# Performance work log

Hardware: AMD Instinct MI355X
Metric: run time of the kernel (lower is better)

Reference implementation:

```python
import jax, jax.numpy as jnp
import numpy as np

D_MODEL = 1024
D_HEAD = 128


def setup_inputs() -> dict:
    key = jax.random.key(0)
    kx, kq, kk, kv, ko = jax.random.split(key, 5)
    x = jax.random.normal(kx, (4, 2048, D_MODEL), dtype=jnp.float32)
    # xavier-uniform-ish init scale
    s_in = (6.0 / (D_MODEL + D_HEAD)) ** 0.5
    wq = jax.random.uniform(kq, (D_MODEL, D_HEAD), minval=-s_in, maxval=s_in, dtype=jnp.float32)
    wk = jax.random.uniform(kk, (D_MODEL, D_HEAD), minval=-s_in, maxval=s_in, dtype=jnp.float32)
    wv = jax.random.uniform(kv, (D_MODEL, D_HEAD), minval=-s_in, maxval=s_in, dtype=jnp.float32)
    wo = jax.random.uniform(ko, (D_HEAD, D_MODEL), minval=-s_in, maxval=s_in, dtype=jnp.float32)
    return {"x": x, "wq": wq, "wk": wk, "wv": wv, "wo": wo}


def reference(x, wq, wk, wv, wo):
    # x: [b, s, d_model]
    s = x.shape[1]
    scale = 1.0 / (D_HEAD ** 0.5)
    q = jnp.einsum('bsd,dh->bsh', x, wq)
    k = jnp.einsum('bsd,dh->bsh', x, wk)
    v = jnp.einsum('bsd,dh->bsh', x, wv)
    scores = jnp.einsum('bqh,bkh->bqk', q, k) * scale  # [b, s, s]
    causal = jnp.tril(jnp.ones((s, s), dtype=bool))
    scores = jnp.where(causal, scores, -jnp.inf)
    attn = jax.nn.softmax(scores, axis=-1)
    ctx = jnp.einsum('bqk,bkh->bqh', attn, v)
    return jnp.einsum('bsh,hd->bsd', ctx, wo)
```

## Files before the change

kernel.cpp:

```cpp
#include <hip/hip_runtime.h>
#include <hip/hip_bf16.h>
#include <math.h>

typedef _Float16 half8 __attribute__((ext_vector_type(8)));
typedef _Float16 half4_t __attribute__((ext_vector_type(4)));
typedef _Float16 half2_t __attribute__((ext_vector_type(2)));
typedef float floatx4 __attribute__((ext_vector_type(4)));
typedef float floatx2 __attribute__((ext_vector_type(2)));

#define MFMA16(a, b, c) __builtin_amdgcn_mfma_f32_16x16x32_f16(a, b, c, 0, 0, 0)
#define MASKVAL (-30000.0f)
#define QSCALE 0.1275261529f

__global__ __launch_bounds__(256) void wprep(
    const float* __restrict__ wq, const float* __restrict__ wk,
    const float* __restrict__ wv, const float* __restrict__ wo,
    _Float16* __restrict__ wqt, _Float16* __restrict__ wkt,
    _Float16* __restrict__ wvt, _Float16* __restrict__ wot) {
  __shared__ float T[32][36];
  int bx = blockIdx.x, tid = threadIdx.x;
  const float* src;
  _Float16* dst;
  int R, C, r0, c0;
  float sc = 1.0f;
  if (bx < 384) {
    int p = bx >> 7, t = bx & 127;
    src = (p == 0) ? wq : (p == 1) ? wk : wv;
    dst = (p == 0) ? wqt : (p == 1) ? wkt : wvt;
    if (p == 0) sc = QSCALE;
    R = 1024; C = 128;
    r0 = (t & 31) * 32; c0 = (t >> 5) * 32;
  } else {
    int t = bx - 384;
    src = wo; dst = wot;
    R = 128; C = 1024;
    r0 = (t & 3) * 32; c0 = (t >> 2) * 32;
  }
  {
    int row = tid >> 3, c4 = (tid & 7) * 4;
    float4 f = *(const float4*)&src[(size_t)(r0 + row) * C + c0 + c4];
    T[row][c4] = f.x; T[row][c4 + 1] = f.y; T[row][c4 + 2] = f.z; T[row][c4 + 3] = f.w;
  }
  __syncthreads();
  {
    int cc = tid >> 3, r4 = (tid & 7) * 4;
    half4_t h;
    h[0] = (_Float16)(T[r4 + 0][cc] * sc);
    h[1] = (_Float16)(T[r4 + 1][cc] * sc);
    h[2] = (_Float16)(T[r4 + 2][cc] * sc);
    h[3] = (_Float16)(T[r4 + 3][cc] * sc);
    *(half4_t*)&dst[(size_t)(c0 + cc) * R + r0 + r4] = h;
  }
}

__global__ __launch_bounds__(256) void qkv_gemm(
    const float* __restrict__ x, const _Float16* __restrict__ wqt,
    const _Float16* __restrict__ wkt, const _Float16* __restrict__ wvt,
    _Float16* __restrict__ Qh, _Float16* __restrict__ Kh,
    _Float16* __restrict__ Vt) {
  __shared__ _Float16 A_lds[32 * 72];
  __shared__ _Float16 B_lds[128 * 72];
  int tid = threadIdx.x;
  int w = tid >> 6, lane = tid & 63, quad = lane >> 4, l16 = lane & 15;
  int m0 = blockIdx.x * 32;
  int proj = blockIdx.y;
  const _Float16* wt = (proj == 0) ? wqt : (proj == 1) ? wkt : wvt;
  floatx4 zero = {0.f, 0.f, 0.f, 0.f};
  floatx4 acc[4];
#pragma unroll
  for (int t = 0; t < 4; t++) acc[t] = zero;

  int arow = tid >> 3, ak8 = (tid & 7) * 8;
  int brow = tid >> 1, bk32 = (tid & 1) * 32;
  int mw = (w >> 1) * 16, nw = (w & 1) * 64;

  for (int k0 = 0; k0 < 1024; k0 += 64) {
    {
      const float* s = x + (size_t)(m0 + arow) * 1024 + k0 + ak8;
      float4 f0 = *(const float4*)(s);
      float4 f1 = *(const float4*)(s + 4);
      half8 h;
      h[0] = (_Float16)f0.x; h[1] = (_Float16)f0.y; h[2] = (_Float16)f0.z; h[3] = (_Float16)f0.w;
      h[4] = (_Float16)f1.x; h[5] = (_Float16)f1.y; h[6] = (_Float16)f1.z; h[7] = (_Float16)f1.w;
      *(half8*)&A_lds[arow * 72 + ak8] = h;
    }
#pragma unroll
    for (int i = 0; i < 4; i++)
      *(half8*)&B_lds[brow * 72 + bk32 + i * 8] =
          *(const half8*)&wt[(size_t)brow * 1024 + k0 + bk32 + i * 8];
    __syncthreads();
    half8 a[2];
#pragma unroll
    for (int c = 0; c < 2; c++)
      a[c] = *(const half8*)&A_lds[(mw + l16) * 72 + c * 32 + quad * 8];
#pragma unroll
    for (int t = 0; t < 4; t++)
#pragma unroll
      for (int c = 0; c < 2; c++) {
        half8 b = *(const half8*)&B_lds[(nw + t * 16 + l16) * 72 + c * 32 + quad * 8];
        acc[t] = MFMA16(a[c], b, acc[t]);
      }
    __syncthreads();
  }
#pragma unroll
  for (int t = 0; t < 4; t++)
#pragma unroll
    for (int r = 0; r < 4; r++) {
      int row = m0 + mw + quad * 4 + r;
      int col = nw + t * 16 + l16;
      _Float16 v = (_Float16)acc[t][r];
      if (proj == 0)
        Qh[(size_t)row * 128 + col] = v;
      else if (proj == 1)
        Kh[(size_t)row * 128 + col] = v;
      else {
        int bb = row >> 11, s = row & 2047;
        Vt[((size_t)(bb * 128 + col)) * 2048 + s] = v;
      }
    }
}

__global__ __launch_bounds__(256, 3) void attn_partial(
    const _Float16* __restrict__ Qh, const _Float16* __restrict__ Kh,
    const _Float16* __restrict__ Vt, _Float16* __restrict__ Opart,
    float* __restrict__ Ml) {
  __shared__ _Float16 KV_lds[128 * 136];
  __shared__ _Float16 P_lds[4 * 16 * 136];
  int tid = threadIdx.x;
  int w = tid >> 6, lane = tid & 63, quad = lane >> 4, l16 = lane & 15;
  int g = (int)blockIdx.x;
  int b = g & 3;
  int r = 271 - (g >> 2);
  int m = (int)sqrtf((float)r + 1.0f);
  while (m * (m + 1) > r) m--;
  while ((m + 1) * (m + 2) <= r) m++;
  int s1 = (m + 1) * (m + 1);
  int qt, kc;
  if (r >= s1) { qt = 2 * m + 1; kc = r - s1; }
  else         { qt = 2 * m;     kc = r - m * (m + 1); }
  int q0 = qt * 64, k0 = kc * 128;
  int qw0 = q0 + w * 16;
  int sidx = (b * 32 + qt) * 16 + kc;

  const _Float16* Kb = Kh + (size_t)b * 2048 * 128;
  const _Float16* Vb = Vt + (size_t)b * 128 * 2048;

  int srow = tid >> 1, scol = (tid & 1) * 64;
#pragma unroll
  for (int i = 0; i < 8; i++)
    *(half8*)&KV_lds[srow * 136 + scol + i * 8] =
        *(const half8*)&Kb[(size_t)(k0 + srow) * 128 + scol + i * 8];
  half8 vreg[8];
#pragma unroll
  for (int i = 0; i < 8; i++)
    vreg[i] = *(const half8*)&Vb[(size_t)srow * 2048 + k0 + scol + i * 8];

  half8 aq[4];
  {
    const _Float16* qbase = Qh + (size_t)(b * 2048 + qw0 + l16) * 128;
#pragma unroll
    for (int c = 0; c < 4; c++) aq[c] = *(const half8*)&qbase[c * 32 + quad * 8];
  }
  __syncthreads();

  floatx4 zero = {0.f, 0.f, 0.f, 0.f};
  floatx4 sa[8];
#pragma unroll
  for (int t = 0; t < 8; t++) sa[t] = zero;
#pragma unroll
  for (int t = 0; t < 8; t++)
#pragma unroll
    for (int c = 0; c < 4; c++) {
      half8 bk = *(const half8*)&KV_lds[(t * 16 + l16) * 136 + c * 32 + quad * 8];
      sa[t] = MFMA16(aq[c], bk, sa[t]);
    }

  float m_r[4], l_r[4];
#pragma unroll
  for (int r2 = 0; r2 < 4; r2++) {
    int query = qw0 + quad * 4 + r2;
    float mx = MASKVAL;
#pragma unroll
    for (int t = 0; t < 8; t++) {
      float s = (k0 + t * 16 + l16 > query) ? MASKVAL : sa[t][r2];
      sa[t][r2] = s;
      mx = fmaxf(mx, s);
    }
#pragma unroll
    for (int off = 1; off < 16; off <<= 1) mx = fmaxf(mx, __shfl_xor(mx, off));
    float rs = 0.f;
#pragma unroll
    for (int t = 0; t < 8; t++) {
      float e = exp2f(sa[t][r2] - mx);
      sa[t][r2] = e;
      rs += e;
    }
#pragma unroll
    for (int off = 1; off < 16; off <<= 1) rs += __shfl_xor(rs, off);
    m_r[r2] = mx;
    l_r[r2] = rs;
  }

  __syncthreads();

#pragma unroll
  for (int i = 0; i < 8; i++)
    *(half8*)&KV_lds[srow * 136 + scol + i * 8] = vreg[i];
  _Float16* P = P_lds + w * 16 * 136;
#pragma unroll
  for (int r2 = 0; r2 < 4; r2++)
#pragma unroll
    for (int t = 0; t < 8; t++)
      P[(quad * 4 + r2) * 136 + t * 16 + l16] = (_Float16)sa[t][r2];
  __syncthreads();

  floatx4 O[8];
#pragma unroll
  for (int t = 0; t < 8; t++) O[t] = zero;
#pragma unroll
  for (int c2 = 0; c2 < 4; c2++) {
    half8 ap = *(const half8*)&P[l16 * 136 + c2 * 32 + quad * 8];
#pragma unroll
    for (int t = 0; t < 8; t++) {
      half8 bv = *(const half8*)&KV_lds[(t * 16 + l16) * 136 + c2 * 32 + quad * 8];
      O[t] = MFMA16(ap, bv, O[t]);
    }
  }

  size_t obase = (size_t)sidx * 8192;
#pragma unroll
  for (int t = 0; t < 8; t++)
#pragma unroll
    for (int r2 = 0; r2 < 4; r2++)
      Opart[obase + (size_t)(w * 16 + quad * 4 + r2) * 128 + t * 16 + l16] = (_Float16)O[t][r2];
  if (l16 == 0)
#pragma unroll
    for (int r2 = 0; r2 < 4; r2++) {
      int row = w * 16 + quad * 4 + r2;
      floatx2 ml;
      ml[0] = m_r[r2];
      ml[1] = l_r[r2];
      *(floatx2*)&Ml[(size_t)sidx * 128 + row * 2] = ml;
    }
}

__global__ __launch_bounds__(256) void attn_combine(
    const _Float16* __restrict__ Opart, const float* __restrict__ Ml,
    _Float16* __restrict__ ctx) {
  int tid = threadIdx.x;
  int w = tid >> 6, lane = tid & 63;
  int row = blockIdx.x * 4 + w;
  int b = row >> 11, s = row & 2047;
  int qt = s >> 6, ri = s & 63;
  int nkc = (qt + 2) >> 1;
  int sidx0 = (b * 32 + qt) * 16;
  float M = MASKVAL;
  for (int i = 0; i < nkc; i++)
    M = fmaxf(M, Ml[(size_t)(sidx0 + i) * 128 + ri * 2]);
  float L = 0.f, a0 = 0.f, a1 = 0.f;
  for (int i = 0; i < nkc; i++) {
    float mi = Ml[(size_t)(sidx0 + i) * 128 + ri * 2];
    float li = Ml[(size_t)(sidx0 + i) * 128 + ri * 2 + 1];
    float sc = exp2f(mi - M);
    L += li * sc;
    half2_t o = *(const half2_t*)&Opart[(size_t)(sidx0 + i) * 8192 + (size_t)ri * 128 + lane * 2];
    a0 += sc * (float)o[0];
    a1 += sc * (float)o[1];
  }
  float inv = 1.f / L;
  half2_t hv;
  hv[0] = (_Float16)(a0 * inv);
  hv[1] = (_Float16)(a1 * inv);
  *(half2_t*)&ctx[(size_t)row * 128 + lane * 2] = hv;
}

__global__ __launch_bounds__(256) void out_gemm(
    const _Float16* __restrict__ ctx, const _Float16* __restrict__ wot,
    float* __restrict__ out) {
  __shared__ _Float16 A_lds[64 * 136];
  __shared__ _Float16 B_lds[128 * 136];
  int tid = threadIdx.x;
  int w = tid >> 6, lane = tid & 63, quad = lane >> 4, l16 = lane & 15;
  int m0 = blockIdx.x * 64, n0 = blockIdx.y * 128;
  {
    int row = tid >> 2, kk = (tid & 3) * 32;
#pragma unroll
    for (int i = 0; i < 4; i++)
      *(half8*)&A_lds[row * 136 + kk + i * 8] =
          *(const half8*)&ctx[(size_t)(m0 + row) * 128 + kk + i * 8];
  }
  {
    int n = tid >> 1, kk = (tid & 1) * 64;
#pragma unroll
    for (int i = 0; i < 8; i++)
      *(half8*)&B_lds[n * 136 + kk + i * 8] =
          *(const half8*)&wot[(size_t)(n0 + n) * 128 + kk + i * 8];
  }
  __syncthreads();
  floatx4 zero = {0.f, 0.f, 0.f, 0.f};
  floatx4 acc[8];
#pragma unroll
  for (int t = 0; t < 8; t++) acc[t] = zero;
  half8 a[4];
#pragma unroll
  for (int c = 0; c < 4; c++) a[c] = *(const half8*)&A_lds[(w * 16 + l16) * 136 + c * 32 + quad * 8];
#pragma unroll
  for (int t = 0; t < 8; t++)
#pragma unroll
    for (int c = 0; c < 4; c++) {
      half8 b = *(const half8*)&B_lds[(t * 16 + l16) * 136 + c * 32 + quad * 8];
      acc[t] = MFMA16(a[c], b, acc[t]);
    }
#pragma unroll
  for (int t = 0; t < 8; t++)
#pragma unroll
    for (int r = 0; r < 4; r++) {
      int row = m0 + w * 16 + quad * 4 + r;
      out[(size_t)row * 1024 + n0 + t * 16 + l16] = acc[t][r];
    }
}

extern "C" void kernel_launch(void* const* d_in, const int* in_sizes, int n_in,
                              void* d_out, int out_size, void* d_ws, size_t ws_size,
                              hipStream_t stream) {
  const float* x = (const float*)d_in[0];
  const float* wq = (const float*)d_in[1];
  const float* wk = (const float*)d_in[2];
  const float* wv = (const float*)d_in[3];
  const float* wo = (const float*)d_in[4];
  char* ws = (char*)d_ws;
  _Float16* wqt = (_Float16*)(ws + 0);
  _Float16* wkt = (_Float16*)(ws + 262144);
  _Float16* wvt = (_Float16*)(ws + 524288);
  _Float16* wot = (_Float16*)(ws + 786432);
  _Float16* Qh  = (_Float16*)(ws + 1048576);
  _Float16* Kh  = (_Float16*)(ws + 3145728);
  _Float16* Vt  = (_Float16*)(ws + 5242880);
  _Float16* ctxh = (_Float16*)(ws + 7340032);
  _Float16* Opart = (_Float16*)(ws + 9437184);
  float* Ml = (float*)(ws + 42991616);
  float* out = (float*)d_out;

  wprep<<<512, 256, 0, stream>>>(wq, wk, wv, wo, wqt, wkt, wvt, wot);
  qkv_gemm<<<dim3(256, 3), 256, 0, stream>>>(x, wqt, wkt, wvt, Qh, Kh, Vt);
  attn_partial<<<1088, 256, 0, stream>>>(Qh, Kh, Vt, Opart, Ml);
  attn_combine<<<2048, 256, 0, stream>>>(Opart, Ml, ctxh);
  out_gemm<<<dim3(128, 8), 256, 0, stream>>>(ctxh, wot, out);
}
```

Before: 164.3 us.

## Prefetch next K-tile into registers and double K-step in QKV GEMM

The QKV projection GEMM now loads the next 128-wide K slice of x and the weights into registers while MFMAs run on the current LDS tile, instead of loading synchronously before each step. The K step grows from 64 to 128, which halves the number of barrier pairs, and a min-blocks-per-CU hint of 3 is added. This raises register pressure and LDS use per block, which may reduce occupancy.

```diff
diff --git a/kernel.cpp b/kernel.cpp
--- a/kernel.cpp
+++ b/kernel.cpp
@@ -53,13 +53,13 @@
   }
 }
 
-__global__ __launch_bounds__(256) void qkv_gemm(
+__global__ __launch_bounds__(256, 3) void qkv_gemm(
     const float* __restrict__ x, const _Float16* __restrict__ wqt,
     const _Float16* __restrict__ wkt, const _Float16* __restrict__ wvt,
     _Float16* __restrict__ Qh, _Float16* __restrict__ Kh,
     _Float16* __restrict__ Vt) {
-  __shared__ _Float16 A_lds[32 * 72];
-  __shared__ _Float16 B_lds[128 * 72];
+  __shared__ _Float16 A_lds[32 * 136];
+  __shared__ _Float16 B_lds[128 * 136];
   int tid = threadIdx.x;
   int w = tid >> 6, lane = tid & 63, quad = lane >> 4, l16 = lane & 15;
   int m0 = blockIdx.x * 32;
@@ -70,34 +70,57 @@
 #pragma unroll
   for (int t = 0; t < 4; t++) acc[t] = zero;
 
-  int arow = tid >> 3, ak8 = (tid & 7) * 8;
-  int brow = tid >> 1, bk32 = (tid & 1) * 32;
+  int arow = tid >> 3, ac0 = (tid & 7) * 16;
+  int brow = tid >> 1, bc0 = (tid & 1) * 64;
   int mw = (w >> 1) * 16, nw = (w & 1) * 64;
 
-  for (int k0 = 0; k0 < 1024; k0 += 64) {
+  const float* asrc = x + (size_t)(m0 + arow) * 1024 + ac0;
+  const _Float16* bsrc = wt + (size_t)brow * 1024 + bc0;
+
+  float4 af[4];
+  half8 bf[8];
+#pragma unroll
+  for (int i = 0; i < 4; i++) af[i] = ((const float4*)asrc)[i];
+#pragma unroll
+  for (int i = 0; i < 8; i++) bf[i] = ((const half8*)bsrc)[i];
+
+  for (int k0 = 0; k0 < 1024; k0 += 128) {
     {
-      const float* s = x + (size_t)(m0 + arow) * 1024 + k0 + ak8;
-      float4 f0 = *(const float4*)(s);
-      float4 f1 = *(const float4*)(s + 4);
-      half8 h;
-      h[0] = (_Float16)f0.x; h[1] = (_Float16)f0.y; h[2] = (_Float16)f0.z; h[3] = (_Float16)f0.w;
-      h[4] = (_Float16)f1.x; h[5] = (_Float16)f1.y; h[6] = (_Float16)f1.z; h[7] = (_Float16)f1.w;
-      *(half8*)&A_lds[arow * 72 + ak8] = h;
-    }
-#pragma unroll
-    for (int i = 0; i < 4; i++)
-      *(half8*)&B_lds[brow * 72 + bk32 + i * 8] =
-          *(const half8*)&wt[(size_t)brow * 1024 + k0 + bk32 + i * 8];
+      half8 h0, h1;
+      h0[0] = (_Float16)af[0].x; h0[1] = (_Float16)af[0].y;
+      h0[2] = (_Float16)af[0].z; h0[3] = (_Float16)af[0].w;
+      h0[4] = (_Float16)af[1].x; h0[5] = (_Float16)af[1].y;
+      h0[6] = (_Float16)af[1].z; h0[7] = (_Float16)af[1].w;
+      h1[0] = (_Float16)af[2].x; h1[1] = (_Float16)af[2].y;
+      h1[2] = (_Float16)af[2].z; h1[3] = (_Float16)af[2].w;
+      h1[4] = (_Float16)af[3].x; h1[5] = (_Float16)af[3].y;
+      h1[6] = (_Float16)af[3].z; h1[7] = (_Float16)af[3].w;
+      *(half8*)&A_lds[arow * 136 + ac0] = h0;
+      *(half8*)&A_lds[arow * 136 + ac0 + 8] = h1;
+    }
+#pragma unroll
+    for (int i = 0; i < 8; i++)
+      *(half8*)&B_lds[brow * 136 + bc0 + i * 8] = bf[i];
     __syncthreads();
-    half8 a[2];
-#pragma unroll
-    for (int c = 0; c < 2; c++)
-      a[c] = *(const half8*)&A_lds[(mw + l16) * 72 + c * 32 + quad * 8];
+
+    if (k0 + 128 < 1024) {
+      const float* a2 = asrc + k0 + 128;
+      const _Float16* b2 = bsrc + k0 + 128;
+#pragma unroll
+      for (int i = 0; i < 4; i++) af[i] = ((const float4*)a2)[i];
+#pragma unroll
+      for (int i = 0; i < 8; i++) bf[i] = ((const half8*)b2)[i];
+    }
+
+    half8 a[4];
+#pragma unroll
+    for (int c = 0; c < 4; c++)
+      a[c] = *(const half8*)&A_lds[(mw + l16) * 136 + c * 32 + quad * 8];
 #pragma unroll
     for (int t = 0; t < 4; t++)
 #pragma unroll
-      for (int c = 0; c < 2; c++) {
-        half8 b = *(const half8*)&B_lds[(nw + t * 16 + l16) * 72 + c * 32 + quad * 8];
+      for (int c = 0; c < 4; c++) {
+        half8 b = *(const half8*)&B_lds[(nw + t * 16 + l16) * 136 + c * 32 + quad * 8];
         acc[t] = MFMA16(a[c], b, acc[t]);
       }
     __syncthreads();
```

Result: faster. 160.3 us (-2.4%).
